# Optimization experiments

Hardware: AMD Instinct MI355X
Metric: run time of the kernel (lower is better)

The kernel has to match this reference:

```python
import jax, jax.numpy as jnp
import numpy as np
from jax import lax

V, D, H, C = 32000, 300, 300, 3
B, T = 128, 512


def setup_inputs() -> dict:
    key = jax.random.key(0)
    ks = jax.random.split(key, 8)
    sentence_ids = jax.random.randint(ks[0], (B, T), 0, V, dtype=jnp.int32)
    lengths = jnp.maximum(jax.random.randint(ks[1], (B,), 0, T, dtype=jnp.int32), 1)
    labels = jax.random.randint(ks[2], (B,), 0, C, dtype=jnp.int32)
    embedding = jax.random.normal(ks[3], (V, D), jnp.float32) * 0.1
    W_lstm = jax.random.normal(ks[4], (D + H, 4 * H), jnp.float32) * 0.05
    b_lstm = jnp.zeros((4 * H,), jnp.float32)
    W_dense = jax.random.normal(ks[5], (H, C), jnp.float32) * 0.05
    b_dense = jnp.zeros((C,), jnp.float32)
    return {"sentence_ids": sentence_ids, "lengths": lengths, "labels": labels,
            "embedding": embedding, "W_lstm": W_lstm, "b_lstm": b_lstm,
            "W_dense": W_dense, "b_dense": b_dense}


def reference(sentence_ids, lengths, labels, embedding, W_lstm, b_lstm, W_dense, b_dense):
    # Embedding lookup: [B, T, D]
    x = embedding[sentence_ids]
    b, t, d = x.shape
    h_units = W_dense.shape[0]
    FORGET_BIAS = 1.0  # TF BasicLSTMCell default

    xs = jnp.swapaxes(x, 0, 1)                                   # [T, B, D]
    step_mask = (jnp.arange(t)[:, None] < lengths[None, :])      # [T, B]

    def step(carry, inp):
        h, c = carry
        xt, m = inp                                              # [B,D], [B]
        z = jnp.concatenate([xt, h], axis=-1) @ W_lstm + b_lstm  # [B, 4H]
        i, j, f, o = jnp.split(z, 4, axis=-1)
        new_c = c * jax.nn.sigmoid(f + FORGET_BIAS) + jax.nn.sigmoid(i) * jnp.tanh(j)
        new_h = jnp.tanh(new_c) * jax.nn.sigmoid(o)
        mm = m[:, None]
        # dynamic_rnn: freeze state past each sequence's length
        h = jnp.where(mm, new_h, h)
        c = jnp.where(mm, new_c, c)
        return (h, c), None

    h0 = jnp.zeros((b, h_units), x.dtype)
    c0 = jnp.zeros((b, h_units), x.dtype)
    (h_final, _), _ = lax.scan(step, (h0, c0), (xs, step_mask))

    logits = h_final @ W_dense + b_dense                          # [B, C]
    logp = jax.nn.log_softmax(logits, axis=-1)
    nll = -jnp.take_along_axis(logp, labels[:, None].astype(jnp.int32), axis=1)[:, 0]
    loss = jnp.mean(nll)
    return loss, logits
```

## Files before the change

### kernel.cpp

```cpp
#include <hip/hip_runtime.h>
#include <hip/hip_bf16.h>
#include <math.h>

#define VV   32000
#define DD   300
#define HU   300
#define NC   3
#define BB   128
#define TT   512
#define N4H  1200
#define CHUNK 64
#define NCHUNK (TT / CHUNK)

#define GC   15
#define GR   16
#define RPW  8
#define UPW  20
#define KSW  96
#define HLB_STRIDE 312
#define HLB_SIZE   (16 * HLB_STRIDE + 32)

static constexpr size_t ZX_F   = (size_t)BB * CHUNK * N4H;
static constexpr size_t EX_W   = (size_t)2 * GR * RPW * HU;
static constexpr size_t CST_F  = (size_t)BB * HU;
static constexpr size_t HFIN_F = (size_t)BB * HU;

typedef __attribute__((ext_vector_type(8))) short bf16x8;
typedef __attribute__((ext_vector_type(8))) _Float16 f16x8;
typedef __attribute__((ext_vector_type(4))) float f32x4;
typedef unsigned long long ull;

__device__ __forceinline__ short f2bf(float f) {
    unsigned u = __float_as_uint(f);
    u += 0x7fff + ((u >> 16) & 1);
    return (short)(u >> 16);
}
__device__ __forceinline__ short f2h(float f) {
    _Float16 h = (_Float16)f;
    return *(short*)&h;
}
__device__ __forceinline__ float h2f(short s) {
    _Float16 h = *(_Float16*)&s;
    return (float)h;
}
__device__ __forceinline__ float sigm(float x) { return 1.f / (1.f + __expf(-x)); }
__device__ __forceinline__ float tanh_(float x) { return 1.f - 2.f / (__expf(2.f * x) + 1.f); }

__global__ void init_kernel(ull* __restrict__ ex, float* __restrict__ cst,
                            float* __restrict__ out) {
    size_t i = (size_t)blockIdx.x * 256 + threadIdx.x;
    if (i < EX_W) ex[i] = 0ull;
    if (i < CST_F) cst[i] = 0.f;
    if (i == 0) out[0] = 0.f;
}

__global__ __launch_bounds__(256) void zx_gemm(
    const float* __restrict__ emb, const int* __restrict__ ids,
    const float* __restrict__ Wl, const float* __restrict__ bl,
    float* __restrict__ zx, int t0)
{
    __shared__ short A_l[256 * 40];
    __shared__ short B_l[80 * 40];
    __shared__ int   ids_l[256];

    const int tid = threadIdx.x;
    const int m0  = blockIdx.x * 256;
    const int n0  = blockIdx.y * 80;
    const int wv  = tid >> 6, ln = tid & 63;

    {
        int m = m0 + tid;
        int b = m >> 6, tc = m & (CHUNK - 1);
        ids_l[tid] = ids[b * TT + t0 + tc];
    }

    f32x4 acc[4][5];
    for (int i = 0; i < 4; ++i)
        for (int j = 0; j < 5; ++j)
            acc[i][j] = (f32x4){0.f, 0.f, 0.f, 0.f};

    for (int k0 = 0; k0 < 320; k0 += 32) {
        __syncthreads();
        {
            const float* src = emb + (size_t)ids_l[tid] * DD;
            #pragma unroll
            for (int q = 0; q < 8; ++q) {
                int kg = k0 + q * 4;
                float4 v;
                if (kg < DD) v = *(const float4*)(src + kg);
                else         v = make_float4(0.f, 0.f, 0.f, 0.f);
                short4 s; s.x = f2bf(v.x); s.y = f2bf(v.y); s.z = f2bf(v.z); s.w = f2bf(v.w);
                *(short4*)&A_l[tid * 40 + q * 4] = s;
            }
        }
        {
            int kk = tid >> 3;
            int c0 = (tid & 7) * 10;
            int kg = k0 + kk;
            #pragma unroll
            for (int c = 0; c < 10; ++c) {
                float v = (kg < DD) ? Wl[(size_t)kg * N4H + n0 + c0 + c] : 0.f;
                B_l[(c0 + c) * 40 + kk] = f2bf(v);
            }
        }
        __syncthreads();
        const int koff = (ln >> 4) * 8;
        bf16x8 afr[4], bfr[5];
        #pragma unroll
        for (int mt = 0; mt < 4; ++mt) {
            int row = wv * 64 + mt * 16 + (ln & 15);
            afr[mt] = *(const bf16x8*)&A_l[row * 40 + koff];
        }
        #pragma unroll
        for (int nt = 0; nt < 5; ++nt) {
            int col = nt * 16 + (ln & 15);
            bfr[nt] = *(const bf16x8*)&B_l[col * 40 + koff];
        }
        #pragma unroll
        for (int mt = 0; mt < 4; ++mt)
            #pragma unroll
            for (int nt = 0; nt < 5; ++nt)
                acc[mt][nt] = __builtin_amdgcn_mfma_f32_16x16x32_bf16(
                    afr[mt], bfr[nt], acc[mt][nt], 0, 0, 0);
    }
    #pragma unroll
    for (int mt = 0; mt < 4; ++mt) {
        #pragma unroll
        for (int nt = 0; nt < 5; ++nt) {
            #pragma unroll
            for (int rg = 0; rg < 4; ++rg) {
                int row = m0 + wv * 64 + mt * 16 + (ln >> 4) * 4 + rg;
                int col = n0 + nt * 16 + (ln & 15);
                zx[(size_t)row * N4H + col] = acc[mt][nt][rg] + bl[col];
            }
        }
    }
}

__global__ __launch_bounds__(256, 1) void lstm_rec(
    const float* __restrict__ zx, const float* __restrict__ Wl,
    const int* __restrict__ lens, ull* __restrict__ ex,
    float* __restrict__ cst, float* __restrict__ hfin, int t0)
{
    const int tid = threadIdx.x;
    const int wv  = tid >> 6, ln = tid & 63;
    const int rg  = blockIdx.x % GR;
    const int cgi = blockIdx.x / GR;
    const int r0  = rg * RPW;
    const int u0  = cgi * UPW;
    const int m   = ln & 15;
    const int quad = ln >> 4;

    const int pstart_tbl[4] = {0, 4, 9, 14};
    const int np_tbl[4]     = {5, 6, 6, 1};
    const int pstart = pstart_tbl[wv];
    const int np     = np_tbl[wv];

    __shared__ short h_hi[HLB_SIZE];
    __shared__ short h_lo[HLB_SIZE];
    __shared__ float zp[2][4][RPW][84];
    __shared__ short w_l[4 * 15 * 64 * 8];

    #pragma unroll
    for (int s = 0; s < 3; ++s) {
        #pragma unroll
        for (int nt = 0; nt < 5; ++nt) {
            int c    = nt * 16 + m;
            int gate = c / 20;
            int wcol = 300 * gate + u0 + (c % 20);
            f16x8 b;
            #pragma unroll
            for (int j = 0; j < 8; ++j) {
                int k = KSW * wv + 32 * s + quad * 8 + j;
                float v = (k < HU) ? Wl[(size_t)(DD + k) * N4H + wcol] : 0.f;
                b[j] = (_Float16)v;
            }
            *(f16x8*)&w_l[(((wv * 15) + (s * 5 + nt)) * 64 + ln) * 8] = b;
        }
    }
    const int nks = (wv == 3) ? 1 : 3;

    for (int i = tid; i < HLB_SIZE; i += 256) { h_hi[i] = 0; h_lo[i] = 0; }

    const int g_u = tid % UPW, g_r = tid / UPW;
    const bool gl = (tid < RPW * UPW);
    float c_reg = 0.f, ho_reg = 0.f;
    int mylen = 0;
    if (gl) {
        c_reg = cst[(size_t)(r0 + g_r) * HU + u0 + g_u];
        mylen = lens[r0 + g_r];
        if (t0 > 0) {
            ull v = __hip_atomic_load(
                ex + (((size_t)(t0 & 1) * GR + rg) * RPW + g_r) * HU + u0 + g_u,
                __ATOMIC_RELAXED, __HIP_MEMORY_SCOPE_AGENT);
            unsigned d = (unsigned)v;
            ho_reg = h2f((short)(d & 0xFFFFu)) + h2f((short)(d >> 16));
        }
    }
    __syncthreads();

    for (int tc = 0; tc < CHUNK; ++tc) {
        const int t = t0 + tc;
        const int par = t & 1;

        float z_pre[4];
        if (gl) {
            const float* zrow = zx + ((size_t)(r0 + g_r) * CHUNK + tc) * N4H;
            #pragma unroll
            for (int gg = 0; gg < 4; ++gg)
                z_pre[gg] = zrow[300 * gg + u0 + g_u];
        }

        if (t > 0) {
            const ull* exb = ex + ((size_t)par * GR + rg) * (RPW * HU);

            if (ln < np) {
                const ull* sp = exb + (pstart + ln) * UPW;
                while ((int)(__hip_atomic_load(sp, __ATOMIC_RELAXED,
                             __HIP_MEMORY_SCOPE_AGENT) >> 32) < t)
                    __builtin_amdgcn_s_sleep(1);
            }

            if (wv < 3) {
                unsigned pend = 0xFFFu;
                do {
                    ull v[12];
                    #pragma unroll
                    for (int k = 0; k < 12; ++k)
                        if ((pend >> k) & 1) {
                            int i = ln + (k << 6);
                            int r = i / 96, u = KSW * wv + (i % 96);
                            v[k] = __hip_atomic_load(exb + r * HU + u,
                                                     __ATOMIC_RELAXED,
                                                     __HIP_MEMORY_SCOPE_AGENT);
                        }
                    unsigned got = 0;
                    #pragma unroll
                    for (int k = 0; k < 12; ++k) {
                        if (((pend >> k) & 1) && (int)(v[k] >> 32) >= t) {
                            int i = ln + (k << 6);
                            int r = i / 96, u = KSW * wv + (i % 96);
                            int idx = r * HLB_STRIDE + u;
                            unsigned d = (unsigned)v[k];
                            h_hi[idx] = (short)(d & 0xFFFFu);
                            h_lo[idx] = (short)(d >> 16);
                            got |= 1u << k;
                        }
                    }
                    pend &= ~got;
                    if (pend) __builtin_amdgcn_s_sleep(1);
                } while (pend);
            } else {
                unsigned pend = (ln < 32) ? 0x3u : 0x1u;
                do {
                    ull v[2];
                    #pragma unroll
                    for (int k = 0; k < 2; ++k)
                        if ((pend >> k) & 1) {
                            int i = ln + (k << 6);
                            int r = i / 12, u = 288 + (i % 12);
                            v[k] = __hip_atomic_load(exb + r * HU + u,
                                                     __ATOMIC_RELAXED,
                                                     __HIP_MEMORY_SCOPE_AGENT);
                        }
                    unsigned got = 0;
                    #pragma unroll
                    for (int k = 0; k < 2; ++k) {
                        if (((pend >> k) & 1) && (int)(v[k] >> 32) >= t) {
                            int i = ln + (k << 6);
                            int r = i / 12, u = 288 + (i % 12);
                            int idx = r * HLB_STRIDE + u;
                            unsigned d = (unsigned)v[k];
                            h_hi[idx] = (short)(d & 0xFFFFu);
                            h_lo[idx] = (short)(d >> 16);
                            got |= 1u << k;
                        }
                    }
                    pend &= ~got;
                    if (pend) __builtin_amdgcn_s_sleep(1);
                } while (pend);
            }
        }

        f32x4 acc[5];
        #pragma unroll
        for (int nt = 0; nt < 5; ++nt) acc[nt] = (f32x4){0.f, 0.f, 0.f, 0.f};
        for (int s = 0; s < nks; ++s) {
            const int aoff = m * HLB_STRIDE + KSW * wv + 32 * s + quad * 8;
            f16x8 ah = *(const f16x8*)&h_hi[aoff];
            f16x8 al = *(const f16x8*)&h_lo[aoff];
            f16x8 bfr[5];
            #pragma unroll
            for (int nt = 0; nt < 5; ++nt)
                bfr[nt] = *(const f16x8*)&w_l[(((wv * 15) + (s * 5 + nt)) * 64 + ln) * 8];
            #pragma unroll
            for (int nt = 0; nt < 5; ++nt)
                acc[nt] = __builtin_amdgcn_mfma_f32_16x16x32_f16(
                    ah, bfr[nt], acc[nt], 0, 0, 0);
            #pragma unroll
            for (int nt = 0; nt < 5; ++nt)
                acc[nt] = __builtin_amdgcn_mfma_f32_16x16x32_f16(
                    al, bfr[nt], acc[nt], 0, 0, 0);
        }
        if (ln < 32) {
            #pragma unroll
            for (int nt = 0; nt < 5; ++nt)
                #pragma unroll
                for (int r4 = 0; r4 < 4; ++r4)
                    zp[par][wv][quad * 4 + r4][nt * 16 + m] = acc[nt][r4];
        }
        __syncthreads();

        if (gl) {
            const int b = r0 + g_r;
            float z4[4];
            #pragma unroll
            for (int gg = 0; gg < 4; ++gg) {
                int cidx = gg * UPW + g_u;
                z4[gg] = z_pre[gg] + zp[par][0][g_r][cidx] + zp[par][1][g_r][cidx]
                                   + zp[par][2][g_r][cidx] + zp[par][3][g_r][cidx];
            }
            float ig = sigm(z4[0]);
            float jg = tanh_(z4[1]);
            float fg = sigm(z4[2] + 1.0f);
            float og = sigm(z4[3]);
            float c_new = c_reg * fg + ig * jg;
            float h_new = tanh_(c_new) * og;
            bool upd = (t < mylen);
            ho_reg = upd ? h_new : ho_reg;
            c_reg  = upd ? c_new : c_reg;
            short hhi = f2h(ho_reg);
            short hlo = f2h(ho_reg - h2f(hhi));
            ull pk = ((ull)(unsigned)(t + 1) << 32)
                   | ((ull)(unsigned short)hlo << 16) | (ull)(unsigned short)hhi;
            __hip_atomic_store(
                ex + (((size_t)((t + 1) & 1) * GR + rg) * RPW + g_r) * HU + u0 + g_u,
                pk, __ATOMIC_RELAXED, __HIP_MEMORY_SCOPE_AGENT);
            if (tc == CHUNK - 1) hfin[(size_t)b * HU + u0 + g_u] = ho_reg;
        }
    }
    if (gl) cst[(size_t)(r0 + g_r) * HU + u0 + g_u] = c_reg;
}

__global__ __launch_bounds__(64) void cls_kernel(
    const float* __restrict__ hfin, const float* __restrict__ Wd,
    const float* __restrict__ bd, const int* __restrict__ labels,
    float* __restrict__ out)
{
    const int b = blockIdx.x;
    const int ln = threadIdx.x;
    const float* h = hfin + (size_t)b * HU;
    float p0 = 0.f, p1 = 0.f, p2 = 0.f;
    for (int k = ln; k < HU; k += 64) {
        float hv = h[k];
        p0 += hv * Wd[k * 3 + 0];
        p1 += hv * Wd[k * 3 + 1];
        p2 += hv * Wd[k * 3 + 2];
    }
    #pragma unroll
    for (int off = 32; off > 0; off >>= 1) {
        p0 += __shfl_down(p0, off);
        p1 += __shfl_down(p1, off);
        p2 += __shfl_down(p2, off);
    }
    if (ln == 0) {
        float l0 = p0 + bd[0], l1 = p1 + bd[1], l2 = p2 + bd[2];
        float m = fmaxf(l0, fmaxf(l1, l2));
        float lse = m + logf(__expf(l0 - m) + __expf(l1 - m) + __expf(l2 - m));
        int lab = labels[b];
        float sel = (lab == 0) ? l0 : ((lab == 1) ? l1 : l2);
        float nll = lse - sel;
        out[1 + b * 3 + 0] = l0;
        out[1 + b * 3 + 1] = l1;
        out[1 + b * 3 + 2] = l2;
        atomicAdd(out, nll * (1.0f / BB));
    }
}

extern "C" void kernel_launch(void* const* d_in, const int* in_sizes, int n_in,
                              void* d_out, int out_size, void* d_ws, size_t ws_size,
                              hipStream_t stream) {
    const int*   ids  = (const int*)d_in[0];
    const int*   lens = (const int*)d_in[1];
    const int*   labs = (const int*)d_in[2];
    const float* emb  = (const float*)d_in[3];
    const float* Wl   = (const float*)d_in[4];
    const float* bl   = (const float*)d_in[5];
    const float* Wd   = (const float*)d_in[6];
    const float* bd   = (const float*)d_in[7];
    float* out = (float*)d_out;

    float* zx   = (float*)d_ws;
    ull*   ex   = (ull*)(zx + ZX_F);
    float* cst  = (float*)(ex + EX_W);
    float* hfin = cst + CST_F;

    {
        int n = (int)((EX_W + 255) / 256);
        init_kernel<<<n, 256, 0, stream>>>(ex, cst, out);
    }
    for (int c = 0; c < NCHUNK; ++c) {
        int t0 = c * CHUNK;
        zx_gemm<<<dim3(32, 15), 256, 0, stream>>>(emb, ids, Wl, bl, zx, t0);
        lstm_rec<<<GR * GC, 256, 0, stream>>>(zx, Wl, lens, ex, cst, hfin, t0);
    }
    cls_kernel<<<BB, 64, 0, stream>>>(hfin, Wd, bd, labs, out);
}
```

Baseline: 2.284 ms.

## Pre-convert embedding table and transposed LSTM weights to bf16 before input GEMM

Adds a prep kernel that converts the full embedding table to padded bf16 rows and writes a transposed, padded bf16 copy of the input part of W_lstm. The input-projection GEMM then copies bf16 rows into shared memory and reads weight fragments straight from global memory, dropping per-tile fp32-to-bf16 conversion and the B shared tile. This removes conversion work that was repeated across the 15 column blocks. In exchange it converts the whole vocabulary every call and needs extra workspace.

New measurement: 2.226 ms. -2.6%, faster.

```diff
diff --git a/kernel.cpp b/kernel.cpp
--- a/kernel.cpp
+++ b/kernel.cpp
@@ -20,10 +20,12 @@
 #define HLB_STRIDE 312
 #define HLB_SIZE   (16 * HLB_STRIDE + 32)
 
-static constexpr size_t ZX_F   = (size_t)BB * CHUNK * N4H;
-static constexpr size_t EX_W   = (size_t)2 * GR * RPW * HU;
-static constexpr size_t CST_F  = (size_t)BB * HU;
-static constexpr size_t HFIN_F = (size_t)BB * HU;
+static constexpr size_t ZX_F    = (size_t)BB * CHUNK * N4H;
+static constexpr size_t EX_W    = (size_t)2 * GR * RPW * HU;
+static constexpr size_t CST_F   = (size_t)BB * HU;
+static constexpr size_t HFIN_F  = (size_t)BB * HU;
+static constexpr size_t EMB16_W = (size_t)VV * 320;
+static constexpr size_t WT_W    = (size_t)N4H * 320;
 
 typedef __attribute__((ext_vector_type(8))) short bf16x8;
 typedef __attribute__((ext_vector_type(8))) _Float16 f16x8;
@@ -54,25 +56,62 @@
     if (i == 0) out[0] = 0.f;
 }
 
+__global__ void prep_kernel(const float* __restrict__ emb,
+                            const float* __restrict__ Wl,
+                            short* __restrict__ emb16, short* __restrict__ wt) {
+    const int NE = VV * 40;
+    const int NW = N4H * 40;
+    for (int j = blockIdx.x * 256 + threadIdx.x; j < NE + NW;
+         j += gridDim.x * 256) {
+        if (j < NE) {
+            int v = j / 40, kb = (j % 40) * 8;
+            bf16x8 o;
+            if (kb + 8 <= DD) {
+                const float* s = emb + (size_t)v * DD + kb;
+                float4 a = *(const float4*)s, b = *(const float4*)(s + 4);
+                o[0] = f2bf(a.x); o[1] = f2bf(a.y); o[2] = f2bf(a.z); o[3] = f2bf(a.w);
+                o[4] = f2bf(b.x); o[5] = f2bf(b.y); o[6] = f2bf(b.z); o[7] = f2bf(b.w);
+            } else {
+                #pragma unroll
+                for (int e = 0; e < 8; ++e) {
+                    int k = kb + e;
+                    o[e] = (k < DD) ? f2bf(emb[(size_t)v * DD + k]) : (short)0;
+                }
+            }
+            *(bf16x8*)&emb16[(size_t)v * 320 + kb] = o;
+        } else {
+            int jj = j - NE;
+            int col = jj / 40, kb = (jj % 40) * 8;
+            bf16x8 o;
+            #pragma unroll
+            for (int e = 0; e < 8; ++e) {
+                int k = kb + e;
+                o[e] = (k < DD) ? f2bf(Wl[(size_t)k * N4H + col]) : (short)0;
+            }
+            *(bf16x8*)&wt[(size_t)col * 320 + kb] = o;
+        }
+    }
+}
+
 __global__ __launch_bounds__(256) void zx_gemm(
-    const float* __restrict__ emb, const int* __restrict__ ids,
-    const float* __restrict__ Wl, const float* __restrict__ bl,
+    const short* __restrict__ emb16, const int* __restrict__ ids,
+    const short* __restrict__ wt, const float* __restrict__ bl,
     float* __restrict__ zx, int t0)
 {
     __shared__ short A_l[256 * 40];
-    __shared__ short B_l[80 * 40];
-    __shared__ int   ids_l[256];
 
     const int tid = threadIdx.x;
     const int m0  = blockIdx.x * 256;
     const int n0  = blockIdx.y * 80;
     const int wv  = tid >> 6, ln = tid & 63;
 
+    int myid;
     {
         int m = m0 + tid;
         int b = m >> 6, tc = m & (CHUNK - 1);
-        ids_l[tid] = ids[b * TT + t0 + tc];
-    }
+        myid = ids[b * TT + t0 + tc];
+    }
+    const short* arow = emb16 + (size_t)myid * 320;
 
     f32x4 acc[4][5];
     for (int i = 0; i < 4; ++i)
@@ -82,26 +121,10 @@
     for (int k0 = 0; k0 < 320; k0 += 32) {
         __syncthreads();
         {
-            const float* src = emb + (size_t)ids_l[tid] * DD;
-            #pragma unroll
-            for (int q = 0; q < 8; ++q) {
-                int kg = k0 + q * 4;
-                float4 v;
-                if (kg < DD) v = *(const float4*)(src + kg);
-                else         v = make_float4(0.f, 0.f, 0.f, 0.f);
-                short4 s; s.x = f2bf(v.x); s.y = f2bf(v.y); s.z = f2bf(v.z); s.w = f2bf(v.w);
-                *(short4*)&A_l[tid * 40 + q * 4] = s;
-            }
-        }
-        {
-            int kk = tid >> 3;
-            int c0 = (tid & 7) * 10;
-            int kg = k0 + kk;
-            #pragma unroll
-            for (int c = 0; c < 10; ++c) {
-                float v = (kg < DD) ? Wl[(size_t)kg * N4H + n0 + c0 + c] : 0.f;
-                B_l[(c0 + c) * 40 + kk] = f2bf(v);
-            }
+            #pragma unroll
+            for (int q = 0; q < 4; ++q)
+                *(bf16x8*)&A_l[tid * 40 + q * 8] =
+                    *(const bf16x8*)(arow + k0 + q * 8);
         }
         __syncthreads();
         const int koff = (ln >> 4) * 8;
@@ -113,8 +136,8 @@
         }
         #pragma unroll
         for (int nt = 0; nt < 5; ++nt) {
-            int col = nt * 16 + (ln & 15);
-            bfr[nt] = *(const bf16x8*)&B_l[col * 40 + koff];
+            int col = n0 + nt * 16 + (ln & 15);
+            bfr[nt] = *(const bf16x8*)&wt[(size_t)col * 320 + k0 + koff];
         }
         #pragma unroll
         for (int mt = 0; mt < 4; ++mt)
@@ -390,18 +413,22 @@
     const float* bd   = (const float*)d_in[7];
     float* out = (float*)d_out;
 
-    float* zx   = (float*)d_ws;
-    ull*   ex   = (ull*)(zx + ZX_F);
-    float* cst  = (float*)(ex + EX_W);
-    float* hfin = cst + CST_F;
+    float* zx    = (float*)d_ws;
+    ull*   ex    = (ull*)(zx + ZX_F);
+    float* cst   = (float*)(ex + EX_W);
+    float* hfin  = cst + CST_F;
+    short* emb16 = (short*)(hfin + HFIN_F);
+    short* wt    = emb16 + EMB16_W;
 
     {
         int n = (int)((EX_W + 255) / 256);
         init_kernel<<<n, 256, 0, stream>>>(ex, cst, out);
     }
+    prep_kernel<<<2048, 256, 0, stream>>>(emb, Wl, emb16, wt);
+
     for (int c = 0; c < NCHUNK; ++c) {
         int t0 = c * CHUNK;
-        zx_gemm<<<dim3(32, 15), 256, 0, stream>>>(emb, ids, Wl, bl, zx, t0);
+        zx_gemm<<<dim3(32, 15), 256, 0, stream>>>(emb16, ids, wt, bl, zx, t0);
         lstm_rec<<<GR * GC, 256, 0, stream>>>(zx, Wl, lens, ex, cst, hfin, t0);
     }
     cls_kernel<<<BB, 64, 0, stream>>>(hfin, Wd, bd, labs, out);
```
